# Kernel tuning notes

Hardware: AMD Instinct MI355X
Metric: run time of the kernel (lower is better)

## Reference

```python
import jax, jax.numpy as jnp
import numpy as np

B, S, D, V, ND = 8, 512, 1024, 32000, 8


def setup_inputs() -> dict:
    key = jax.random.key(0)
    k1, k2, k3, k4 = jax.random.split(key, 4)
    scale = 0.02
    return {
        "hidden_states": jax.random.normal(k1, (B, S, D), dtype=jnp.float32),
        "domain_ids": jax.random.randint(k2, (B,), 0, ND + 1),  # index ND triggers default head
        "W_base": jax.random.normal(k3, (D, D), dtype=jnp.float32) * scale,
        "b_base": jnp.zeros((D,), dtype=jnp.float32),
        # slots 0..ND-1 are domain heads, slot ND is the default head
        "W_heads": jax.random.normal(k4, (ND + 1, D, V), dtype=jnp.float32) * scale,
        "b_heads": jnp.zeros((ND + 1, V), dtype=jnp.float32),
    }


def reference(hidden_states, domain_ids, W_base, b_base, W_heads, b_heads):
    # base_projection: Linear(D, D)
    hidden = jnp.einsum("bsd,de->bse", hidden_states, W_base) + b_base
    num_domains = W_heads.shape[0] - 1
    # out-of-range domain ids fall back to the default head (last slot)
    idx = jnp.where((domain_ids >= 0) & (domain_ids < num_domains), domain_ids, num_domains)
    Wg = W_heads[idx]              # [B, D, V] gathered per-example head weights
    bg = b_heads[idx]              # [B, V]
    out = jnp.einsum("bsd,bdv->bsv", hidden, Wg) + bg[:, None, :]
    return out
```

## Files before the change

### kernel.cpp

```cpp
#include <hip/hip_runtime.h>
#include <hip/hip_bf16.h>


#define BCNT 8
#define SLEN 512
#define DDIM 1024
#define VDIM 32000
#define NDOM 8

typedef __attribute__((ext_vector_type(4))) float f32x4;
typedef __attribute__((ext_vector_type(8))) short bf16x8;

static __device__ __forceinline__ unsigned short f2bf(float f) {
    union { float f; unsigned int u; } x; x.f = f;
    unsigned int u = x.u;
    return (unsigned short)((u + 0x7FFFu + ((u >> 16) & 1u)) >> 16);
}

static __device__ __forceinline__ unsigned int pack2(float lo, float hi) {
    float2 t; t.x = lo; t.y = hi;
    union { __hip_bfloat162 h; unsigned int u; } c;
    c.h = __float22bfloat162_rn(t);
    return c.u;
}

#define SBAR()   __builtin_amdgcn_s_barrier()
#define SCHED0() __builtin_amdgcn_sched_barrier(0)

__global__ __launch_bounds__(256)
void gemm1_k(const float* __restrict__ Af, const float* __restrict__ Bbase,
             const float* __restrict__ bias, __hip_bfloat16* __restrict__ Cb,
             int Mrows)
{
    __shared__ __align__(16) __hip_bfloat16 lds_a[128 * 64];
    __shared__ __align__(16) unsigned int   lds_b[32 * 128];

    const int tid  = threadIdx.x;
    const int lane = tid & 63;
    const int w    = tid >> 6;

    const int nwg = gridDim.x;
    const int bid = blockIdx.x;
    const int q   = nwg >> 3;
    const int sid = (bid & 7) * q + (bid >> 3);

    const int MT = Mrows >> 7;
    const int mt = sid % MT;
    const int nt = sid / MT;
    const int m0 = mt << 7;
    const int n0 = nt << 7;

    f32x4 acc[4][4];
    #pragma unroll
    for (int m = 0; m < 4; ++m)
        #pragma unroll
        for (int n = 0; n < 4; ++n)
            acc[m][n] = (f32x4)0.0f;

    const int wr = w >> 1, wc = w & 1;
    const int lr = lane & 15, lg = lane >> 4;

    for (int kt = 0; kt < DDIM / 64; ++kt) {
        const int kbase = kt * 64;

        #pragma unroll
        for (int t = 0; t < 8; ++t) {
            const int flat = (t * 256 + tid) * 4;
            const int row = flat >> 6, col = flat & 63;
            const float4 v = *(const float4*)(Af + (size_t)(m0 + row) * DDIM + kbase + col);
            uint2 pp;
            pp.x = pack2(v.x, v.y);
            pp.y = pack2(v.z, v.w);
            *(uint2*)(lds_a + flat) = pp;
        }

        #pragma unroll
        for (int t = 0; t < 4; ++t) {
            const int id = t * 256 + tid;
            const int kk = id >> 5;
            const int n  = (id & 31) << 2;
            const float* b0 = Bbase + (size_t)(kbase + 2 * kk) * DDIM + n0 + n;
            const float4 e = *(const float4*)b0;
            const float4 o = *(const float4*)(b0 + DDIM);
            uint4 pw;
            pw.x = pack2(e.x, o.x);
            pw.y = pack2(e.y, o.y);
            pw.z = pack2(e.z, o.z);
            pw.w = pack2(e.w, o.w);
            const int ns = n ^ ((kk & 4) << 2);
            *(uint4*)&lds_b[kk * 128 + ns] = pw;
        }

        __syncthreads();

        #pragma unroll
        for (int ks = 0; ks < 2; ++ks) {
            bf16x8 af[4], bfr[4];
            #pragma unroll
            for (int m = 0; m < 4; ++m) {
                const int row = wr * 64 + m * 16 + lr;
                const int k   = ks * 32 + lg * 8;
                af[m] = *(const bf16x8*)&lds_a[row * 64 + k];
            }
            #pragma unroll
            for (int n = 0; n < 4; ++n) {
                const int col = wc * 64 + n * 16 + lr;
                const int kkb = ks * 16 + lg * 4;
                union { unsigned int u[4]; bf16x8 v; } cvt;
                #pragma unroll
                for (int j = 0; j < 4; ++j) {
                    const int kk = kkb + j;
                    const int ns = col ^ ((kk & 4) << 2);
                    cvt.u[j] = lds_b[kk * 128 + ns];
                }
                bfr[n] = cvt.v;
            }
            #pragma unroll
            for (int m = 0; m < 4; ++m)
                #pragma unroll
                for (int n = 0; n < 4; ++n)
                    acc[m][n] = __builtin_amdgcn_mfma_f32_16x16x32_bf16(af[m], bfr[n], acc[m][n], 0, 0, 0);
        }

        __syncthreads();
    }

    #pragma unroll
    for (int m = 0; m < 4; ++m) {
        #pragma unroll
        for (int n = 0; n < 4; ++n) {
            const int col = n0 + wc * 64 + n * 16 + lr;
            const float bv = bias[col];
            #pragma unroll
            for (int r = 0; r < 4; ++r) {
                const int row = m0 + wr * 64 + m * 16 + lg * 4 + r;
                Cb[(size_t)row * DDIM + col] = __hip_bfloat16_raw{f2bf(acc[m][n][r] + bv)};
            }
        }
    }
}

__global__ __launch_bounds__(256, 3)
void gemm2_k(const __hip_bfloat16* __restrict__ A, const float* __restrict__ Wh,
             const float* __restrict__ bh, float* __restrict__ out,
             const int* __restrict__ dom)
{
    __shared__ __align__(16) __hip_bfloat16 ldsA[128 * 64];
    __shared__ __align__(16) unsigned int   ldsB[128 * 32];

    const int tid  = threadIdx.x;
    const int lane = tid & 63;
    const int w    = tid >> 6;
    const int wr   = w >> 1;
    const int wc   = w & 1;
    const int lr   = lane & 15;
    const int lg   = lane >> 4;

    const int bid  = blockIdx.x;
    const int q    = gridDim.x >> 3;
    const int sid  = (bid & 7) * q + (bid >> 3);
    const int mt   = sid & 3;
    const int rest = sid >> 2;
    const int nt   = rest % 250;
    const int ex   = rest / 250;
    const int m0   = ex * SLEN + mt * 128;
    const int n0   = nt * 128;

    const int di  = dom[ex];
    const int hid = (di >= 0 && di < NDOM) ? di : NDOM;
    const float* Bp   = Wh + (size_t)hid * DDIM * (size_t)VDIM;
    const float* bias = bh + (size_t)hid * (size_t)VDIM;

    f32x4 acc[4][4];
    #pragma unroll
    for (int m = 0; m < 4; ++m)
        #pragma unroll
        for (int n = 0; n < 4; ++n)
            acc[m][n] = (f32x4)0.0f;

    const int nb4 = (tid & 31) << 2;
    const int kb  = (tid >> 5) << 3;
    const int qb  = kb >> 1;

    f32x4 br4[8];

    #define LOADB(KT) do {                                                         \
        const float* _p = Bp + (size_t)((KT) * 64 + kb) * VDIM + n0 + nb4;         \
        _Pragma("unroll")                                                          \
        for (int j = 0; j < 8; ++j) br4[j] = *(const f32x4*)(_p + (size_t)j * VDIM); \
    } while (0)

    #define WRITEB() do {                                                          \
        _Pragma("unroll")                                                          \
        for (int i = 0; i < 4; ++i) {                                              \
            const int col  = nb4 + i;                                              \
            const int slot = qb ^ (((col >> 1) & 7) << 2);                         \
            uint4 wv;                                                              \
            wv.x = pack2(br4[0][i], br4[1][i]);                                    \
            wv.y = pack2(br4[2][i], br4[3][i]);                                    \
            wv.z = pack2(br4[4][i], br4[5][i]);                                    \
            wv.w = pack2(br4[6][i], br4[7][i]);                                    \
            *(uint4*)&ldsB[col * 32 + slot] = wv;                                  \
        }                                                                          \
    } while (0)

    #define STAGEA(KT) do {                                                        \
        _Pragma("unroll")                                                          \
        for (int i = 0; i < 4; ++i) {                                              \
            const int base_e = (i * 4 + w) * 512;                                  \
            const int flat   = base_e + lane * 8;                                  \
            const int row    = flat >> 6;                                          \
            const int kbyte  = (flat & 63) * 2;                                    \
            const int srck   = (kbyte ^ ((row & 7) << 4)) >> 1;                    \
            const __hip_bfloat16* src = A + (size_t)(m0 + row) * DDIM + (KT) * 64 + srck; \
            __builtin_amdgcn_global_load_lds(                                      \
                (const __attribute__((address_space(1))) unsigned int*)src,        \
                (__attribute__((address_space(3))) unsigned int*)(ldsA + base_e),  \
                16, 0, 0);                                                         \
        }                                                                          \
    } while (0)

    #define COMPUTE() do {                                                         \
        _Pragma("unroll")                                                          \
        for (int ks = 0; ks < 2; ++ks) {                                           \
            bf16x8 af[4], bfr[4];                                                  \
            _Pragma("unroll")                                                      \
            for (int m = 0; m < 4; ++m) {                                          \
                const int row = wr * 64 + m * 16 + lr;                             \
                const int kby = ks * 64 + lg * 16;                                 \
                const int eff = kby ^ ((row & 7) << 4);                            \
                af[m] = *(const bf16x8*)&ldsA[row * 64 + (eff >> 1)];              \
            }                                                                      \
            _Pragma("unroll")                                                      \
            for (int n = 0; n < 4; ++n) {                                          \
                const int col  = wc * 64 + n * 16 + lr;                            \
                const int kkb  = ks * 16 + lg * 4;                                 \
                const int slot = kkb ^ (((col >> 1) & 7) << 2);                    \
                bfr[n] = *(const bf16x8*)&ldsB[col * 32 + slot];                   \
            }                                                                      \
            _Pragma("unroll")                                                      \
            for (int m = 0; m < 4; ++m)                                            \
                _Pragma("unroll")                                                  \
                for (int n = 0; n < 4; ++n)                                        \
                    acc[m][n] = __builtin_amdgcn_mfma_f32_16x16x32_bf16(af[m], bfr[n], acc[m][n], 0, 0, 0); \
        }                                                                          \
    } while (0)

    LOADB(0);
    SCHED0();
    STAGEA(0);
    SCHED0();
    WRITEB();
    SCHED0();
    LOADB(1);
    SCHED0();
    asm volatile("s_waitcnt vmcnt(8) lgkmcnt(0)" ::: "memory");
    SCHED0();
    SBAR();

    for (int kt = 0; kt < 16; ++kt) {
        COMPUTE();
        if (kt < 15) {
            SCHED0();
            SBAR();
            SCHED0();
            STAGEA(kt + 1);
            SCHED0();
            WRITEB();
            SCHED0();
            if (kt < 14) {
                LOADB(kt + 2);
                SCHED0();
                asm volatile("s_waitcnt vmcnt(8) lgkmcnt(0)" ::: "memory");
            } else {
                asm volatile("s_waitcnt vmcnt(0) lgkmcnt(0)" ::: "memory");
            }
            SCHED0();
            SBAR();
        }
    }

    #pragma unroll
    for (int n = 0; n < 4; ++n) {
        const int col = n0 + wc * 64 + n * 16 + lr;
        const float bv = bias[col];
        #pragma unroll
        for (int m = 0; m < 4; ++m) {
            #pragma unroll
            for (int r = 0; r < 4; ++r) {
                const int row = m0 + wr * 64 + m * 16 + lg * 4 + r;
                out[(size_t)row * VDIM + col] = acc[m][n][r] + bv;
            }
        }
    }

    #undef LOADB
    #undef WRITEB
    #undef STAGEA
    #undef COMPUTE
}

extern "C" void kernel_launch(void* const* d_in, const int* in_sizes, int n_in,
                              void* d_out, int out_size, void* d_ws, size_t ws_size,
                              hipStream_t stream)
{
    const float* hs  = (const float*)d_in[0];
    const int*   dom = (const int*)d_in[1];
    const float* Wb  = (const float*)d_in[2];
    const float* bb  = (const float*)d_in[3];
    const float* Wh  = (const float*)d_in[4];
    const float* bh  = (const float*)d_in[5];
    float* out = (float*)d_out;
    __hip_bfloat16* hidden = (__hip_bfloat16*)d_ws;

    const int M = BCNT * SLEN;

    const int g1 = (M / 128) * (DDIM / 128);
    hipLaunchKernelGGL(gemm1_k, dim3(g1), dim3(256), 0, stream, hs, Wb, bb, hidden, M);

    const int g2 = BCNT * (SLEN / 128) * (VDIM / 128);
    hipLaunchKernelGGL(gemm2_k, dim3(g2), dim3(256), 0, stream, hidden, Wh, bh, out, dom);
}
```

Measured before the change: 538.7 us.

## Load A fragments from global directly and double-buffer B in LDS

The per-head GEMM no longer stages the bf16 hidden activations through LDS. Each wave now loads its A fragments straight from global memory into registers, while the converted B tile goes into two ping-pong LDS buffers, so each k-step needs only one barrier. MFMA blocks are also wrapped in s_setprio to raise wave priority during compute. This removes the A LDS traffic and one barrier per step, and lowers the LDS footprint. In exchange, the A global loads are issued right before use with no prefetch, and the wave pairs sharing rows load the same A data twice.

```diff
diff --git a/kernel.cpp b/kernel.cpp
--- a/kernel.cpp
+++ b/kernel.cpp
@@ -145,8 +145,7 @@
              const float* __restrict__ bh, float* __restrict__ out,
              const int* __restrict__ dom)
 {
-    __shared__ __align__(16) __hip_bfloat16 ldsA[128 * 64];
-    __shared__ __align__(16) unsigned int   ldsB[128 * 32];
+    __shared__ __align__(16) unsigned int ldsB[2][128 * 32];
 
     const int tid  = threadIdx.x;
     const int lane = tid & 63;
@@ -178,6 +177,8 @@
         for (int n = 0; n < 4; ++n)
             acc[m][n] = (f32x4)0.0f;
 
+    const __hip_bfloat16* aRow = A + (size_t)(m0 + wr * 64 + lr) * DDIM + lg * 8;
+
     const int nb4 = (tid & 31) << 2;
     const int kb  = (tid >> 5) << 3;
     const int qb  = kb >> 1;
@@ -190,7 +191,7 @@
         for (int j = 0; j < 8; ++j) br4[j] = *(const f32x4*)(_p + (size_t)j * VDIM); \
     } while (0)
 
-    #define WRITEB() do {                                                          \
+    #define WRITEB(LB) do {                                                        \
         _Pragma("unroll")                                                          \
         for (int i = 0; i < 4; ++i) {                                              \
             const int col  = nb4 + i;                                              \
@@ -200,84 +201,68 @@
             wv.y = pack2(br4[2][i], br4[3][i]);                                    \
             wv.z = pack2(br4[4][i], br4[5][i]);                                    \
             wv.w = pack2(br4[6][i], br4[7][i]);                                    \
-            *(uint4*)&ldsB[col * 32 + slot] = wv;                                  \
+            *(uint4*)&(LB)[col * 32 + slot] = wv;                                  \
         }                                                                          \
     } while (0)
 
-    #define STAGEA(KT) do {                                                        \
-        _Pragma("unroll")                                                          \
-        for (int i = 0; i < 4; ++i) {                                              \
-            const int base_e = (i * 4 + w) * 512;                                  \
-            const int flat   = base_e + lane * 8;                                  \
-            const int row    = flat >> 6;                                          \
-            const int kbyte  = (flat & 63) * 2;                                    \
-            const int srck   = (kbyte ^ ((row & 7) << 4)) >> 1;                    \
-            const __hip_bfloat16* src = A + (size_t)(m0 + row) * DDIM + (KT) * 64 + srck; \
-            __builtin_amdgcn_global_load_lds(                                      \
-                (const __attribute__((address_space(1))) unsigned int*)src,        \
-                (__attribute__((address_space(3))) unsigned int*)(ldsA + base_e),  \
-                16, 0, 0);                                                         \
+    #define READ_AF(AF, KT, KS) do {                                               \
+        _Pragma("unroll")                                                          \
+        for (int m = 0; m < 4; ++m)                                                \
+            AF[m] = *(const bf16x8*)(aRow + (size_t)(m * 16) * DDIM + (KT) * 64 + (KS) * 32); \
+    } while (0)
+
+    #define READ_BF(BF, LB, KS) do {                                               \
+        _Pragma("unroll")                                                          \
+        for (int n = 0; n < 4; ++n) {                                              \
+            const int col  = wc * 64 + n * 16 + lr;                                \
+            const int kkb  = (KS) * 16 + lg * 4;                                   \
+            const int slot = kkb ^ (((col >> 1) & 7) << 2);                        \
+            BF[n] = *(const bf16x8*)&(LB)[col * 32 + slot];                        \
         }                                                                          \
     } while (0)
 
-    #define COMPUTE() do {                                                         \
-        _Pragma("unroll")                                                          \
-        for (int ks = 0; ks < 2; ++ks) {                                           \
-            bf16x8 af[4], bfr[4];                                                  \
+    #define MFMA16(AF, BF) do {                                                    \
+        _Pragma("unroll")                                                          \
+        for (int m = 0; m < 4; ++m)                                                \
             _Pragma("unroll")                                                      \
-            for (int m = 0; m < 4; ++m) {                                          \
-                const int row = wr * 64 + m * 16 + lr;                             \
-                const int kby = ks * 64 + lg * 16;                                 \
-                const int eff = kby ^ ((row & 7) << 4);                            \
-                af[m] = *(const bf16x8*)&ldsA[row * 64 + (eff >> 1)];              \
-            }                                                                      \
-            _Pragma("unroll")                                                      \
-            for (int n = 0; n < 4; ++n) {                                          \
-                const int col  = wc * 64 + n * 16 + lr;                            \
-                const int kkb  = ks * 16 + lg * 4;                                 \
-                const int slot = kkb ^ (((col >> 1) & 7) << 2);                    \
-                bfr[n] = *(const bf16x8*)&ldsB[col * 32 + slot];                   \
-            }                                                                      \
-            _Pragma("unroll")                                                      \
-            for (int m = 0; m < 4; ++m)                                            \
-                _Pragma("unroll")                                                  \
-                for (int n = 0; n < 4; ++n)                                        \
-                    acc[m][n] = __builtin_amdgcn_mfma_f32_16x16x32_bf16(af[m], bfr[n], acc[m][n], 0, 0, 0); \
-        }                                                                          \
+            for (int n = 0; n < 4; ++n)                                            \
+                acc[m][n] = __builtin_amdgcn_mfma_f32_16x16x32_bf16(AF[m], BF[n], acc[m][n], 0, 0, 0); \
     } while (0)
 
     LOADB(0);
     SCHED0();
-    STAGEA(0);
-    SCHED0();
-    WRITEB();
+    WRITEB(ldsB[0]);
     SCHED0();
     LOADB(1);
     SCHED0();
-    asm volatile("s_waitcnt vmcnt(8) lgkmcnt(0)" ::: "memory");
+    asm volatile("s_waitcnt lgkmcnt(0)" ::: "memory");
     SCHED0();
     SBAR();
 
     for (int kt = 0; kt < 16; ++kt) {
-        COMPUTE();
-        if (kt < 15) {
-            SCHED0();
-            SBAR();
-            SCHED0();
-            STAGEA(kt + 1);
-            SCHED0();
-            WRITEB();
-            SCHED0();
-            if (kt < 14) {
-                LOADB(kt + 2);
-                SCHED0();
-                asm volatile("s_waitcnt vmcnt(8) lgkmcnt(0)" ::: "memory");
-            } else {
-                asm volatile("s_waitcnt vmcnt(0) lgkmcnt(0)" ::: "memory");
-            }
-            SCHED0();
-            SBAR();
-        }
+        unsigned int* cur = ldsB[kt & 1];
+        unsigned int* nxt = ldsB[(kt + 1) & 1];
+
+        bf16x8 af[4], bfr[4];
+
+        READ_AF(af, kt, 0);
+        READ_BF(bfr, cur, 0);
+        if (kt < 15) WRITEB(nxt);
+        if (kt < 14) LOADB(kt + 2);
+        SCHED0();
+        __builtin_amdgcn_s_setprio(1);
+        MFMA16(af, bfr);
+        __builtin_amdgcn_s_setprio(0);
+
+        READ_AF(af, kt, 1);
+        READ_BF(bfr, cur, 1);
+        SCHED0();
+        asm volatile("s_waitcnt lgkmcnt(0)" ::: "memory");
+        SCHED0();
+        if (kt < 15) SBAR();
+        __builtin_amdgcn_s_setprio(1);
+        MFMA16(af, bfr);
+        __builtin_amdgcn_s_setprio(0);
     }
 
     #pragma unroll
@@ -296,8 +281,9 @@
 
     #undef LOADB
     #undef WRITEB
-    #undef STAGEA
-    #undef COMPUTE
+    #undef READ_AF
+    #undef READ_BF
+    #undef MFMA16
 }
 
 extern "C" void kernel_launch(void* const* d_in, const int* in_sizes, int n_in,
```

After: 822.4 us. 1.53x slower.
